# Optimization experiments

Measured on AMD Instinct MI355X. Metric: run time of the kernel, lower is better.

Reference implementation:

```python
import jax, jax.numpy as jnp
import numpy as np

N, F, E, G = 100000, 128, 600000, 1000
EPS = 1e-5


def setup_inputs() -> dict:
    key = jax.random.key(0)
    k1, k2, k3, k4 = jax.random.split(key, 4)
    x = jax.random.normal(k1, (N, F), dtype=jnp.float32)
    graph_id = jnp.sort(jax.random.randint(k2, (N,), 0, G, dtype=jnp.int32))
    edge_src = jax.random.randint(k3, (E,), 0, N, dtype=jnp.int32)
    edge_dst = jax.random.randint(k4, (E,), 0, N, dtype=jnp.int32)
    return {
        "x": x,
        "gamma": jnp.ones((F,), jnp.float32),
        "beta": jnp.zeros((F,), jnp.float32),
        "lambda_batch": jnp.ones((F,), jnp.float32),
        "lambda_graph": jnp.ones((F,), jnp.float32),
        "lambda_adja": jnp.ones((F,), jnp.float32),
        "lambda_node": jnp.ones((F,), jnp.float32),
        "graph_id": graph_id,
        "edge_src": edge_src,
        "edge_dst": edge_dst,
    }


def _batch_norm(x):
    # BatchNorm1d in training mode: biased stats over the node (batch) axis.
    mu = jnp.mean(x, axis=0, keepdims=True)
    var = jnp.mean(jnp.square(x), axis=0, keepdims=True) - jnp.square(mu)
    return (x - mu) * jax.lax.rsqrt(var + EPS)


def _graph_norm(x, graph_id):
    # Per-graph mean/var per feature via segment reductions. graph_id: [N]
    ones = jnp.ones((x.shape[0],), x.dtype)
    cnt = jax.ops.segment_sum(ones, graph_id, num_segments=G)  # [G]
    cnt = jnp.maximum(cnt, 1.0)[:, None]
    s = jax.ops.segment_sum(x, graph_id, num_segments=G)               # [G,F]
    s2 = jax.ops.segment_sum(jnp.square(x), graph_id, num_segments=G)  # [G,F]
    mu = s / cnt
    var = jnp.maximum(s2 / cnt - jnp.square(mu), 0.0)
    return (x - mu[graph_id]) * jax.lax.rsqrt(var[graph_id] + EPS)


def _adja_node_norm(x, edge_src, edge_dst):
    # Per-node stats over in-neighbors: normalize x_i with mean/var of {x_j : j->i}.
    msg = x[edge_src]  # [E,F]
    deg = jax.ops.segment_sum(jnp.ones((E,), x.dtype), edge_dst, num_segments=N)
    deg = jnp.maximum(deg, 1.0)[:, None]
    s = jax.ops.segment_sum(msg, edge_dst, num_segments=N)
    s2 = jax.ops.segment_sum(jnp.square(msg), edge_dst, num_segments=N)
    mu = s / deg
    var = jnp.maximum(s2 / deg - jnp.square(mu), 0.0)
    return (x - mu) * jax.lax.rsqrt(var + EPS)


def _node_norm(x):
    # LayerNorm over feature axis, no affine.
    mu = jnp.mean(x, axis=-1, keepdims=True)
    var = jnp.mean(jnp.square(x - mu), axis=-1, keepdims=True)
    return (x - mu) * jax.lax.rsqrt(var + EPS)


def reference(x, gamma, beta, lambda_batch, lambda_graph, lambda_adja,
              lambda_node, graph_id, edge_src, edge_dst):
    x_b = _batch_norm(x)
    x_g = _graph_norm(x, graph_id)
    x_a = _adja_node_norm(x, edge_src, edge_dst)
    x_n = _node_norm(x)
    # norm_lambda(): softmax across the four lambda vectors per feature.
    lam = jax.nn.softmax(jnp.stack([lambda_batch, lambda_graph, lambda_adja,
                                    lambda_node], axis=0), axis=0)  # [4,F]
    x_new = lam[0] * x_b + lam[1] * x_g + lam[2] * x_a + lam[3] * x_n
    return gamma * x_new + beta
```

## Files before the change

### kernel.cpp

```cpp
#include <hip/hip_runtime.h>

#define N_NODES 100000
#define NF      128
#define NE      600000
#define NG      1000
#define EPSF    1e-5f

#define STATS_NB (N_NODES / 32)
#define DEG_NB   (((NE / 4) + 255) / 256)
#define ALLOC_NB ((N_NODES + 255) / 256)
#define BRED_NB  64

typedef float v2f __attribute__((ext_vector_type(2)));

__global__ __launch_bounds__(256) void k1_stats_deg(
    const float* __restrict__ x, const int* __restrict__ gid,
    const int* __restrict__ edst,
    float* __restrict__ gsum, float* __restrict__ gsq, int* __restrict__ cnt,
    int* __restrict__ deg)
{
    if (blockIdx.x >= STATS_NB) {
        int t = (blockIdx.x - STATS_NB) * 256 + threadIdx.x;
        if (t < NE / 4) {
            const int4 d4 = reinterpret_cast<const int4*>(edst)[t];
            atomicAdd(&deg[d4.x], 1);
            atomicAdd(&deg[d4.y], 1);
            atomicAdd(&deg[d4.z], 1);
            atomicAdd(&deg[d4.w], 1);
        }
        return;
    }
    const int wave = threadIdx.x >> 6;
    const int lane = threadIdx.x & 63;
    const int f = lane * 2;
    const int r0 = blockIdx.x * 32 + wave * 8;
    const int r1 = r0 + 8;

    float gsx = 0.f, gsy = 0.f, gqx = 0.f, gqy = 0.f;
    int cur = gid[r0];
    int runStart = r0;

    for (int r = r0; r < r1; ++r) {
        int g = gid[r];
        if (g != cur) {
            atomicAdd(&gsum[cur * NF + f],     gsx);
            atomicAdd(&gsum[cur * NF + f + 1], gsy);
            atomicAdd(&gsq [cur * NF + f],     gqx);
            atomicAdd(&gsq [cur * NF + f + 1], gqy);
            if (lane == 0) atomicAdd(&cnt[cur], r - runStart);
            gsx = gsy = gqx = gqy = 0.f;
            cur = g; runStart = r;
        }
        const float2 v = *reinterpret_cast<const float2*>(x + (size_t)r * NF + f);
        gsx += v.x; gsy += v.y; gqx += v.x * v.x; gqy += v.y * v.y;
    }
    atomicAdd(&gsum[cur * NF + f],     gsx);
    atomicAdd(&gsum[cur * NF + f + 1], gsy);
    atomicAdd(&gsq [cur * NF + f],     gqx);
    atomicAdd(&gsq [cur * NF + f + 1], gqy);
    if (lane == 0) atomicAdd(&cnt[cur], r1 - runStart);
}

__global__ __launch_bounds__(256) void k2_alloc_bred(
    const int* __restrict__ deg, int2* __restrict__ odeg, int* __restrict__ cursor,
    int* __restrict__ total,
    const float* __restrict__ gsum, const float* __restrict__ gsq,
    float* __restrict__ bsum, float* __restrict__ bsq)
{
    if (blockIdx.x < ALLOC_NB) {
        const int i = blockIdx.x * 256 + threadIdx.x;
        const int lane = threadIdx.x & 63;
        int d = (i < N_NODES) ? deg[i] : 0;
        int p = d;
#pragma unroll
        for (int st = 1; st < 64; st <<= 1) {
            int v = __shfl_up(p, st, 64);
            if (lane >= st) p += v;
        }
        int wtot = __shfl(p, 63, 64);
        int base = 0;
        if (lane == 63) base = atomicAdd(total, wtot);
        base = __shfl(base, 63, 64);
        if (i < N_NODES) {
            int o = base + p - d;
            odeg[i] = make_int2(o, d);
            cursor[i] = o;
        }
    } else {
        int b = blockIdx.x - ALLOC_NB;
        int t = threadIdx.x;
        int f = t & 127, gl = t >> 7;
        float s = 0.f, q = 0.f;
#pragma unroll
        for (int k = 0; k < 8; ++k) {
            int g = b * 16 + gl * 8 + k;
            if (g < NG) { s += gsum[g * NF + f]; q += gsq[g * NF + f]; }
        }
        atomicAdd(&bsum[f], s);
        atomicAdd(&bsq[f], q);
    }
}

__global__ __launch_bounds__(256) void k3_fill(
    const int* __restrict__ esrc, const int* __restrict__ edst,
    int* __restrict__ cursor, int* __restrict__ nbr)
{
    int t = blockIdx.x * 256 + threadIdx.x;
    if (t < NE / 4) {
        const int4 d4 = reinterpret_cast<const int4*>(edst)[t];
        const int4 s4 = reinterpret_cast<const int4*>(esrc)[t];
        int p;
        p = atomicAdd(&cursor[d4.x], 1); nbr[p] = s4.x;
        p = atomicAdd(&cursor[d4.y], 1); nbr[p] = s4.y;
        p = atomicAdd(&cursor[d4.z], 1); nbr[p] = s4.z;
        p = atomicAdd(&cursor[d4.w], 1); nbr[p] = s4.w;
    }
}

__global__ __launch_bounds__(256) void k5_final(
    const float* __restrict__ x, const int* __restrict__ gid,
    const float* __restrict__ gsum, const float* __restrict__ gsq,
    const int* __restrict__ cnt,
    const float* __restrict__ bsum, const float* __restrict__ bsq,
    const float* __restrict__ gamma, const float* __restrict__ beta,
    const float* __restrict__ lb, const float* __restrict__ lg,
    const float* __restrict__ la, const float* __restrict__ ln,
    const int2* __restrict__ odeg, const int* __restrict__ nbr,
    float* __restrict__ out)
{
    const int wave = threadIdx.x >> 6;
    const int lane = threadIdx.x & 63;
    const int i = blockIdx.x * 4 + wave;
    const int f = lane * 2;
    const int f1 = f + 1;

    const float2 xi = *reinterpret_cast<const float2*>(x + (size_t)i * NF + f);

    const int2 od = odeg[i];
    const int s0 = od.x, dg = od.y;
    float asx = 0.f, asy = 0.f, aqx = 0.f, aqy = 0.f;
    for (int e = 0; e < dg; e += 8) {
        int idx[8];
#pragma unroll
        for (int k = 0; k < 8; ++k)
            idx[k] = nbr[(e + k < dg) ? (s0 + e + k) : s0];
#pragma unroll
        for (int k = 0; k < 8; ++k) {
            const float2 v = *reinterpret_cast<const float2*>(x + (size_t)idx[k] * NF + f);
            const float m = (e + k < dg) ? 1.f : 0.f;
            asx += m * v.x; asy += m * v.y;
            aqx += m * v.x * v.x; aqy += m * v.y * v.y;
        }
    }

    const float invN = 1.0f / (float)N_NODES;
    float mbx = bsum[f]  * invN, mby = bsum[f1] * invN;
    float vbx = bsq[f]  * invN - mbx * mbx;
    float vby = bsq[f1] * invN - mby * mby;
    float rvbx = rsqrtf(vbx + EPSF), rvby = rsqrtf(vby + EPSF);

    float l0x = lb[f],  l1x = lg[f],  l2x = la[f],  l3x = ln[f];
    float l0y = lb[f1], l1y = lg[f1], l2y = la[f1], l3y = ln[f1];
    float mx = fmaxf(fmaxf(l0x, l1x), fmaxf(l2x, l3x));
    float my = fmaxf(fmaxf(l0y, l1y), fmaxf(l2y, l3y));
    float w0x = __expf(l0x - mx), w1x = __expf(l1x - mx), w2x = __expf(l2x - mx), w3x = __expf(l3x - mx);
    float w0y = __expf(l0y - my), w1y = __expf(l1y - my), w2y = __expf(l2y - my), w3y = __expf(l3y - my);
    float rsx = gamma[f]  / (w0x + w1x + w2x + w3x);
    float rsy = gamma[f1] / (w0y + w1y + w2y + w3y);
    w0x *= rsx; w1x *= rsx; w2x *= rsx; w3x *= rsx;
    w0y *= rsy; w1y *= rsy; w2y *= rsy; w3y *= rsy;
    const float btx = beta[f], bty = beta[f1];

    float xbx = (xi.x - mbx) * rvbx;
    float xby = (xi.y - mby) * rvby;

    const int g = gid[i];
    float c = (float)cnt[g]; if (c < 1.f) c = 1.f;
    float rc = 1.0f / c;
    const float2 gs = *reinterpret_cast<const float2*>(gsum + (size_t)g * NF + f);
    const float2 gq = *reinterpret_cast<const float2*>(gsq  + (size_t)g * NF + f);
    float mgx = gs.x * rc, mgy = gs.y * rc;
    float vgx = gq.x * rc - mgx * mgx; if (vgx < 0.f) vgx = 0.f;
    float vgy = gq.y * rc - mgy * mgy; if (vgy < 0.f) vgy = 0.f;
    float xgx = (xi.x - mgx) * rsqrtf(vgx + EPSF);
    float xgy = (xi.y - mgy) * rsqrtf(vgy + EPSF);

    float s = xi.x + xi.y;
#pragma unroll
    for (int d = 1; d < 64; d <<= 1) s += __shfl_xor(s, d, 64);
    const float mn = s * (1.0f / NF);
    float dxx = xi.x - mn, dyy = xi.y - mn;
    float q = dxx * dxx + dyy * dyy;
#pragma unroll
    for (int d = 1; d < 64; d <<= 1) q += __shfl_xor(q, d, 64);
    const float rvn = rsqrtf(q * (1.0f / NF) + EPSF);
    float xnx = dxx * rvn, xny = dyy * rvn;

    float dgc = (float)dg; if (dgc < 1.f) dgc = 1.f;
    float rdg = 1.0f / dgc;
    float max_ = asx * rdg, may_ = asy * rdg;
    float vax = aqx * rdg - max_ * max_; if (vax < 0.f) vax = 0.f;
    float vay = aqy * rdg - may_ * may_; if (vay < 0.f) vay = 0.f;
    float xax = (xi.x - max_) * rsqrtf(vax + EPSF);
    float xay = (xi.y - may_) * rsqrtf(vay + EPSF);

    v2f o;
    o.x = w0x * xbx + w1x * xgx + w2x * xax + w3x * xnx + btx;
    o.y = w0y * xby + w1y * xgy + w2y * xay + w3y * xny + bty;
    __builtin_nontemporal_store(o, reinterpret_cast<v2f*>(out + (size_t)i * NF + f));
}

extern "C" void kernel_launch(void* const* d_in, const int* in_sizes, int n_in,
                              void* d_out, int out_size, void* d_ws, size_t ws_size,
                              hipStream_t stream) {
    const float* x     = (const float*)d_in[0];
    const float* gamma = (const float*)d_in[1];
    const float* beta  = (const float*)d_in[2];
    const float* lb    = (const float*)d_in[3];
    const float* lg    = (const float*)d_in[4];
    const float* la    = (const float*)d_in[5];
    const float* ln    = (const float*)d_in[6];
    const int*   gid   = (const int*)d_in[7];
    const int*   esrc  = (const int*)d_in[8];
    const int*   edst  = (const int*)d_in[9];
    float*       out   = (float*)d_out;

    float* ws    = (float*)d_ws;
    float* bsum  = ws;
    float* bsq   = bsum + NF;
    float* gsum  = bsq + NF;
    float* gsq   = gsum + (size_t)NG * NF;
    int*   cnt   = (int*)(gsq + (size_t)NG * NF);
    int*   deg   = cnt + NG;
    int*   total = deg + N_NODES;
    int*   cursor= total + 2;
    int2*  odeg  = (int2*)(cursor + N_NODES);
    int*   nbr   = (int*)(odeg + N_NODES);

    const size_t zero_elems = (size_t)2 * NF + (size_t)2 * NG * NF + NG + N_NODES + 2;
    hipMemsetAsync(d_ws, 0, zero_elems * sizeof(float), stream);

    k1_stats_deg<<<STATS_NB + DEG_NB, 256, 0, stream>>>(
        x, gid, edst, gsum, gsq, cnt, deg);
    k2_alloc_bred<<<ALLOC_NB + BRED_NB, 256, 0, stream>>>(
        deg, odeg, cursor, total, gsum, gsq, bsum, bsq);
    k3_fill<<<DEG_NB, 256, 0, stream>>>(esrc, edst, cursor, nbr);
    k5_final<<<N_NODES / 4, 256, 0, stream>>>(
        x, gid, gsum, gsq, cnt, bsum, bsq, gamma, beta, lb, lg, la, ln,
        odeg, nbr, out);
}
```

Before: 290.8 us.

## Precompute per-graph and per-feature norm constants; batch loads in stats and gather

Per-graph mean and rsqrt-variance, batch-norm stats and softmax-lambda weights are now computed once, in extra blocks of the fill kernel, and stored into workspace. The final kernel just loads these constants instead of recomputing them per node. The stats kernel now issues all 8 row loads before accumulating. The neighbor gather loop gains a mask-free fast path for full groups of 8. The output store changes from nontemporal to a plain store, which may affect cache behavior for the large output write.

New measurement: 281.3 us. -3.3%, faster.

```diff
diff --git a/kernel.cpp b/kernel.cpp
--- a/kernel.cpp
+++ b/kernel.cpp
@@ -10,8 +10,7 @@
 #define DEG_NB   (((NE / 4) + 255) / 256)
 #define ALLOC_NB ((N_NODES + 255) / 256)
 #define BRED_NB  64
-
-typedef float v2f __attribute__((ext_vector_type(2)));
+#define PREP_NB  ((NG * NF) / 256 + 1)
 
 __global__ __launch_bounds__(256) void k1_stats_deg(
     const float* __restrict__ x, const int* __restrict__ gid,
@@ -34,31 +33,37 @@
     const int lane = threadIdx.x & 63;
     const int f = lane * 2;
     const int r0 = blockIdx.x * 32 + wave * 8;
-    const int r1 = r0 + 8;
+
+    float2 v[8];
+    int g8[8];
+#pragma unroll
+    for (int k = 0; k < 8; ++k) {
+        v[k] = *reinterpret_cast<const float2*>(x + (size_t)(r0 + k) * NF + f);
+        g8[k] = gid[r0 + k];
+    }
 
     float gsx = 0.f, gsy = 0.f, gqx = 0.f, gqy = 0.f;
-    int cur = gid[r0];
-    int runStart = r0;
-
-    for (int r = r0; r < r1; ++r) {
-        int g = gid[r];
-        if (g != cur) {
+    int cur = g8[0];
+    int runStart = 0;
+#pragma unroll
+    for (int k = 0; k < 8; ++k) {
+        if (g8[k] != cur) {
             atomicAdd(&gsum[cur * NF + f],     gsx);
             atomicAdd(&gsum[cur * NF + f + 1], gsy);
             atomicAdd(&gsq [cur * NF + f],     gqx);
             atomicAdd(&gsq [cur * NF + f + 1], gqy);
-            if (lane == 0) atomicAdd(&cnt[cur], r - runStart);
+            if (lane == 0) atomicAdd(&cnt[cur], k - runStart);
             gsx = gsy = gqx = gqy = 0.f;
-            cur = g; runStart = r;
-        }
-        const float2 v = *reinterpret_cast<const float2*>(x + (size_t)r * NF + f);
-        gsx += v.x; gsy += v.y; gqx += v.x * v.x; gqy += v.y * v.y;
+            cur = g8[k]; runStart = k;
+        }
+        gsx += v[k].x; gsy += v[k].y;
+        gqx += v[k].x * v[k].x; gqy += v[k].y * v[k].y;
     }
     atomicAdd(&gsum[cur * NF + f],     gsx);
     atomicAdd(&gsum[cur * NF + f + 1], gsy);
     atomicAdd(&gsq [cur * NF + f],     gqx);
     atomicAdd(&gsq [cur * NF + f + 1], gqy);
-    if (lane == 0) atomicAdd(&cnt[cur], r1 - runStart);
+    if (lane == 0) atomicAdd(&cnt[cur], 8 - runStart);
 }
 
 __global__ __launch_bounds__(256) void k2_alloc_bred(
@@ -101,45 +106,82 @@
     }
 }
 
-__global__ __launch_bounds__(256) void k3_fill(
+__global__ __launch_bounds__(256) void k3_fill_prep(
     const int* __restrict__ esrc, const int* __restrict__ edst,
-    int* __restrict__ cursor, int* __restrict__ nbr)
-{
-    int t = blockIdx.x * 256 + threadIdx.x;
-    if (t < NE / 4) {
-        const int4 d4 = reinterpret_cast<const int4*>(edst)[t];
-        const int4 s4 = reinterpret_cast<const int4*>(esrc)[t];
-        int p;
-        p = atomicAdd(&cursor[d4.x], 1); nbr[p] = s4.x;
-        p = atomicAdd(&cursor[d4.y], 1); nbr[p] = s4.y;
-        p = atomicAdd(&cursor[d4.z], 1); nbr[p] = s4.z;
-        p = atomicAdd(&cursor[d4.w], 1); nbr[p] = s4.w;
-    }
-}
-
-__global__ __launch_bounds__(256) void k5_final(
-    const float* __restrict__ x, const int* __restrict__ gid,
-    const float* __restrict__ gsum, const float* __restrict__ gsq,
-    const int* __restrict__ cnt,
+    int* __restrict__ cursor, int* __restrict__ nbr,
+    float* __restrict__ gsum, float* __restrict__ gsq, const int* __restrict__ cnt,
     const float* __restrict__ bsum, const float* __restrict__ bsq,
     const float* __restrict__ gamma, const float* __restrict__ beta,
     const float* __restrict__ lb, const float* __restrict__ lg,
     const float* __restrict__ la, const float* __restrict__ ln,
-    const int2* __restrict__ odeg, const int* __restrict__ nbr,
-    float* __restrict__ out)
+    float* __restrict__ fc)
+{
+    if (blockIdx.x < DEG_NB) {
+        int t = blockIdx.x * 256 + threadIdx.x;
+        if (t < NE / 4) {
+            const int4 d4 = reinterpret_cast<const int4*>(edst)[t];
+            const int4 s4 = reinterpret_cast<const int4*>(esrc)[t];
+            int p;
+            p = atomicAdd(&cursor[d4.x], 1); nbr[p] = s4.x;
+            p = atomicAdd(&cursor[d4.y], 1); nbr[p] = s4.y;
+            p = atomicAdd(&cursor[d4.z], 1); nbr[p] = s4.z;
+            p = atomicAdd(&cursor[d4.w], 1); nbr[p] = s4.w;
+        }
+        return;
+    }
+    int b = blockIdx.x - DEG_NB;
+    if (b < (NG * NF) / 256) {
+        int idx = b * 256 + threadIdx.x;
+        int g = idx >> 7;
+        float c = (float)cnt[g]; if (c < 1.f) c = 1.f;
+        float rc = 1.0f / c;
+        float m = gsum[idx] * rc;
+        float v = gsq[idx] * rc - m * m; if (v < 0.f) v = 0.f;
+        gsum[idx] = m;
+        gsq[idx]  = rsqrtf(v + EPSF);
+    } else if (threadIdx.x < NF) {
+        int f = threadIdx.x;
+        float mb = bsum[f] * (1.0f / N_NODES);
+        float vb = bsq[f] * (1.0f / N_NODES) - mb * mb;
+        float rvb = rsqrtf(vb + EPSF);
+        float l0 = lb[f], l1 = lg[f], l2 = la[f], l3 = ln[f];
+        float m = fmaxf(fmaxf(l0, l1), fmaxf(l2, l3));
+        float w0 = __expf(l0 - m), w1 = __expf(l1 - m), w2 = __expf(l2 - m), w3 = __expf(l3 - m);
+        float rs = gamma[f] / (w0 + w1 + w2 + w3);
+        float* p = fc + f * 8;
+        p[0] = mb; p[1] = rvb;
+        p[2] = w0 * rs; p[3] = w1 * rs; p[4] = w2 * rs; p[5] = w3 * rs;
+        p[6] = beta[f]; p[7] = 0.f;
+    }
+}
+
+__global__ __launch_bounds__(256) void k5_final(
+    const float* __restrict__ x, const int* __restrict__ gid,
+    const float* __restrict__ gmu, const float* __restrict__ grs,
+    const float* __restrict__ fc, const int2* __restrict__ odeg,
+    const int* __restrict__ nbr, float* __restrict__ out)
 {
     const int wave = threadIdx.x >> 6;
     const int lane = threadIdx.x & 63;
     const int i = blockIdx.x * 4 + wave;
     const int f = lane * 2;
-    const int f1 = f + 1;
-
-    const float2 xi = *reinterpret_cast<const float2*>(x + (size_t)i * NF + f);
 
     const int2 od = odeg[i];
     const int s0 = od.x, dg = od.y;
     float asx = 0.f, asy = 0.f, aqx = 0.f, aqy = 0.f;
-    for (int e = 0; e < dg; e += 8) {
+    int e = 0;
+    for (; e + 8 <= dg; e += 8) {
+        int idx[8];
+#pragma unroll
+        for (int k = 0; k < 8; ++k) idx[k] = nbr[s0 + e + k];
+#pragma unroll
+        for (int k = 0; k < 8; ++k) {
+            const float2 v = *reinterpret_cast<const float2*>(x + (size_t)idx[k] * NF + f);
+            asx += v.x; asy += v.y;
+            aqx += v.x * v.x; aqy += v.y * v.y;
+        }
+    }
+    if (e < dg) {
         int idx[8];
 #pragma unroll
         for (int k = 0; k < 8; ++k)
@@ -153,37 +195,21 @@
         }
     }
 
-    const float invN = 1.0f / (float)N_NODES;
-    float mbx = bsum[f]  * invN, mby = bsum[f1] * invN;
-    float vbx = bsq[f]  * invN - mbx * mbx;
-    float vby = bsq[f1] * invN - mby * mby;
-    float rvbx = rsqrtf(vbx + EPSF), rvby = rsqrtf(vby + EPSF);
-
-    float l0x = lb[f],  l1x = lg[f],  l2x = la[f],  l3x = ln[f];
-    float l0y = lb[f1], l1y = lg[f1], l2y = la[f1], l3y = ln[f1];
-    float mx = fmaxf(fmaxf(l0x, l1x), fmaxf(l2x, l3x));
-    float my = fmaxf(fmaxf(l0y, l1y), fmaxf(l2y, l3y));
-    float w0x = __expf(l0x - mx), w1x = __expf(l1x - mx), w2x = __expf(l2x - mx), w3x = __expf(l3x - mx);
-    float w0y = __expf(l0y - my), w1y = __expf(l1y - my), w2y = __expf(l2y - my), w3y = __expf(l3y - my);
-    float rsx = gamma[f]  / (w0x + w1x + w2x + w3x);
-    float rsy = gamma[f1] / (w0y + w1y + w2y + w3y);
-    w0x *= rsx; w1x *= rsx; w2x *= rsx; w3x *= rsx;
-    w0y *= rsy; w1y *= rsy; w2y *= rsy; w3y *= rsy;
-    const float btx = beta[f], bty = beta[f1];
-
-    float xbx = (xi.x - mbx) * rvbx;
-    float xby = (xi.y - mby) * rvby;
+    const float2 xi = *reinterpret_cast<const float2*>(x + (size_t)i * NF + f);
+
+    const float4 c0 = *reinterpret_cast<const float4*>(fc + f * 8);
+    const float4 c1 = *reinterpret_cast<const float4*>(fc + f * 8 + 4);
+    const float4 d0 = *reinterpret_cast<const float4*>(fc + (f + 1) * 8);
+    const float4 d1 = *reinterpret_cast<const float4*>(fc + (f + 1) * 8 + 4);
+
+    float xbx = (xi.x - c0.x) * c0.y;
+    float xby = (xi.y - d0.x) * d0.y;
 
     const int g = gid[i];
-    float c = (float)cnt[g]; if (c < 1.f) c = 1.f;
-    float rc = 1.0f / c;
-    const float2 gs = *reinterpret_cast<const float2*>(gsum + (size_t)g * NF + f);
-    const float2 gq = *reinterpret_cast<const float2*>(gsq  + (size_t)g * NF + f);
-    float mgx = gs.x * rc, mgy = gs.y * rc;
-    float vgx = gq.x * rc - mgx * mgx; if (vgx < 0.f) vgx = 0.f;
-    float vgy = gq.y * rc - mgy * mgy; if (vgy < 0.f) vgy = 0.f;
-    float xgx = (xi.x - mgx) * rsqrtf(vgx + EPSF);
-    float xgy = (xi.y - mgy) * rsqrtf(vgy + EPSF);
+    const float2 mg = *reinterpret_cast<const float2*>(gmu + (size_t)g * NF + f);
+    const float2 rg = *reinterpret_cast<const float2*>(grs + (size_t)g * NF + f);
+    float xgx = (xi.x - mg.x) * rg.x;
+    float xgy = (xi.y - mg.y) * rg.y;
 
     float s = xi.x + xi.y;
 #pragma unroll
@@ -204,10 +230,9 @@
     float xax = (xi.x - max_) * rsqrtf(vax + EPSF);
     float xay = (xi.y - may_) * rsqrtf(vay + EPSF);
 
-    v2f o;
-    o.x = w0x * xbx + w1x * xgx + w2x * xax + w3x * xnx + btx;
-    o.y = w0y * xby + w1y * xgy + w2y * xay + w3y * xny + bty;
-    __builtin_nontemporal_store(o, reinterpret_cast<v2f*>(out + (size_t)i * NF + f));
+    float outx = c0.z * xbx + c0.w * xgx + c1.x * xax + c1.y * xnx + c1.z;
+    float outy = d0.z * xby + d0.w * xgy + d1.x * xay + d1.y * xny + d1.z;
+    *reinterpret_cast<float2*>(out + (size_t)i * NF + f) = make_float2(outx, outy);
 }
 
 extern "C" void kernel_launch(void* const* d_in, const int* in_sizes, int n_in,
@@ -236,6 +261,7 @@
     int*   cursor= total + 2;
     int2*  odeg  = (int2*)(cursor + N_NODES);
     int*   nbr   = (int*)(odeg + N_NODES);
+    float* fc    = (float*)(nbr + NE);
 
     const size_t zero_elems = (size_t)2 * NF + (size_t)2 * NG * NF + NG + N_NODES + 2;
     hipMemsetAsync(d_ws, 0, zero_elems * sizeof(float), stream);
@@ -244,8 +270,9 @@
         x, gid, edst, gsum, gsq, cnt, deg);
     k2_alloc_bred<<<ALLOC_NB + BRED_NB, 256, 0, stream>>>(
         deg, odeg, cursor, total, gsum, gsq, bsum, bsq);
-    k3_fill<<<DEG_NB, 256, 0, stream>>>(esrc, edst, cursor, nbr);
+    k3_fill_prep<<<DEG_NB + PREP_NB, 256, 0, stream>>>(
+        esrc, edst, cursor, nbr, gsum, gsq, cnt, bsum, bsq,
+        gamma, beta, lb, lg, la, ln, fc);
     k5_final<<<N_NODES / 4, 256, 0, stream>>>(
-        x, gid, gsum, gsq, cnt, bsum, bsq, gamma, beta, lb, lg, la, ln,
-        odeg, nbr, out);
-}
+        x, gid, gsum, gsq, fc, odeg, nbr, out);
+}
```
